# Performance work log

Measured on AMD Instinct MI355X. Metric: run time of the kernel, lower is better.

## Reference

```python
import jax, jax.numpy as jnp
import numpy as np
import math

K_HISTORY = 32  # sliding-window length over GRU hidden states


def rotate_half(x):
    half = x.shape[-1] // 2
    return jnp.concatenate([-x[..., half:], x[..., :half]], axis=-1)


def setup_inputs() -> dict:
    key = jax.random.key(0)
    ks = jax.random.split(key, 8)
    B, MB, IN = 8, 512, 1024          # batch, max_bin, input_size (gru_hidden_size)
    EMB, H, KVH, HD, BS = 1024, 16, 4, 64, 16  # embed_dim, heads, kv_heads, head_dim, bin_size
    h = jax.random.normal(ks[0], (B, MB, IN), jnp.float32)
    # RoPE tables: rotate-half layout, theta repeated over both halves
    pos = jnp.arange(MB, dtype=jnp.float32)
    inv_freq = 1.0 / (10000.0 ** (jnp.arange(0, HD, 2, dtype=jnp.float32) / HD))
    theta = pos[:, None] * inv_freq[None, :]            # (MB, HD/2)
    theta = jnp.concatenate([theta, theta], axis=-1)    # (MB, HD)
    freqs_cos = jnp.cos(theta)
    freqs_sin = jnp.sin(theta)
    s = 0.02
    Wq = jax.random.normal(ks[1], (EMB, H * HD), jnp.float32) * s
    Wk = jax.random.normal(ks[2], (IN, KVH * HD), jnp.float32) * s
    Wv = jax.random.normal(ks[3], (IN, KVH * HD), jnp.float32) * s
    Wo = jax.random.normal(ks[4], (H * HD, EMB), jnp.float32) * s
    output_queries = jax.random.normal(ks[5], (BS, EMB), jnp.float32)
    Wr = jax.random.normal(ks[6], (EMB, 2), jnp.float32) * s
    br = jnp.zeros((2,), jnp.float32)
    return {"h": h, "freqs_cos": freqs_cos, "freqs_sin": freqs_sin,
            "Wq": Wq, "Wk": Wk, "Wv": Wv, "Wo": Wo,
            "output_queries": output_queries, "Wr": Wr, "br": br}


def reference(h, freqs_cos, freqs_sin, Wq, Wk, Wv, Wo, output_queries, Wr, br):
    B, MB, IN = h.shape
    HD = freqs_cos.shape[1]
    H = Wq.shape[1] // HD
    KVH = Wk.shape[1] // HD
    n_rep = H // KVH
    BS = output_queries.shape[0]
    K = K_HISTORY

    # sliding windows over bins: window t covers h[t-K+1 : t+1] (zero left-pad)
    h_padded = jnp.concatenate([jnp.zeros((B, K - 1, IN), h.dtype), h], axis=1)
    idx = jnp.arange(MB)[:, None] + jnp.arange(K)[None, :]   # (MB, K)
    h_win = h_padded[:, idx, :]                              # (B, MB, K, IN)

    k = (h_win @ Wk).reshape(B, MB, K, KVH, HD)
    v = (h_win @ Wv).reshape(B, MB, K, KVH, HD)

    # queries: shared learned output queries, identical across batch & bins
    q = (output_queries @ Wq).reshape(BS, H, HD)             # (BS, H, HD)
    # RoPE on Q only (is_decoder=True) at within-bin offsets 0..BS-1
    offs = jnp.arange(BS)
    cos = freqs_cos[offs][:, None, :]                        # (BS, 1, HD)
    sin = freqs_sin[offs][:, None, :]
    q = q * cos + rotate_half(q) * sin                       # (BS, H, HD)

    # GQA: repeat_interleave KV heads to H heads
    k = jnp.repeat(k, n_rep, axis=3)                         # (B, MB, K, H, HD)
    v = jnp.repeat(v, n_rep, axis=3)

    scores = jnp.einsum("qhd,bmkhd->bmhqk", q, k) / math.sqrt(HD)
    attn = jax.nn.softmax(scores, axis=-1)                   # (B, MB, H, BS, K)
    attn_out = jnp.einsum("bmhqk,bmkhd->bmqhd", attn, v)
    attn_out = attn_out.reshape(B, MB, BS, H * HD)

    z = attn_out @ Wo                                        # (B, MB, BS, EMB)
    vel = z @ Wr + br                                        # (B, MB, BS, 2)
    return vel.reshape(B, MB * BS, 2)
```

## Files before the change

### kernel.cpp

```cpp
#include <hip/hip_runtime.h>


typedef __attribute__((ext_vector_type(8))) short v8s;
typedef __attribute__((ext_vector_type(4))) float v4f;

#define OFF_WOR  0u
#define OFF_QR   2048u
#define OFF_WTH  18432u
#define OFF_WTL  182272u
#define OFF_S0   346112u
#define OFF_S1   1460224u
#define OFF_VW0  2574336u
#define OFF_VW1  2713600u

#define SROW 544

__device__ __forceinline__ void split_bf16(float a, unsigned short& h, unsigned short& l) {
    const unsigned u = __float_as_uint(a);
    h = (unsigned short)(u >> 16);
    const float r = a - __uint_as_float(u & 0xFFFF0000u);
    unsigned v = __float_as_uint(r);
    v += 0x7FFFu + ((v >> 16) & 1u);
    l = (unsigned short)(v >> 16);
}

__global__ __launch_bounds__(256) void kP(
    const float* __restrict__ oq, const float* __restrict__ Wq,
    const float* __restrict__ fc, const float* __restrict__ fs,
    const float* __restrict__ Wo, const float* __restrict__ Wr,
    float* __restrict__ qr, float* __restrict__ Wor,
    float* __restrict__ S0, float* __restrict__ S1,
    float* __restrict__ VW0, float* __restrict__ VW1,
    unsigned* __restrict__ wthu, unsigned* __restrict__ wtlu)
{
    __shared__ float sm[2048];
    const int b = blockIdx.x, t = threadIdx.x;
    if (b < 256) {
        const int q = b >> 4, h = b & 15;
        #pragma unroll
        for (int j = 0; j < 4; ++j) sm[t + 256 * j] = oq[q * 1024 + t + 256 * j];
        __syncthreads();
        const int w = t >> 6, lane = t & 63;
        const float* wq = Wq + (size_t)(w * 256) * 1024 + h * 64 + lane;
        const float* os = sm + w * 256;
        float acc = 0.f;
        #pragma unroll 8
        for (int e = 0; e < 256; ++e) acc = fmaf(os[e], wq[(size_t)e * 1024], acc);
        sm[1024 + w * 64 + lane] = acc;
        __syncthreads();
        if (t < 64) {
            const int d = t, p = d ^ 32;
            const float a1 = sm[1024 + d] + sm[1088 + d] + sm[1152 + d] + sm[1216 + d];
            const float a2 = sm[1024 + p] + sm[1088 + p] + sm[1152 + p] + sm[1216 + p];
            const float c = fc[q * 64 + d], s = fs[q * 64 + d];
            const float rh = (d < 32) ? -a2 : a2;
            qr[q * 1024 + h * 64 + d] = fmaf(a1, c, rh * s);
        }
    } else if (b < 512) {
        #pragma unroll
        for (int j = 0; j < 8; ++j) sm[t + 256 * j] = Wr[t + 256 * j];
        __syncthreads();
        const int i = (b - 256) * 4 + (t >> 6);
        const int lane = t & 63;
        float a0 = 0.f, a1 = 0.f;
        const float* wo = Wo + (size_t)i * 1024 + lane;
        #pragma unroll
        for (int j = 0; j < 16; ++j) {
            const float w = wo[j * 64];
            const int e = lane + j * 64;
            a0 = fmaf(w, sm[2 * e], a0);
            a1 = fmaf(w, sm[2 * e + 1], a1);
        }
        #pragma unroll
        for (int w = 1; w < 64; w <<= 1) {
            a0 += __shfl_xor(a0, w, 64);
            a1 += __shfl_xor(a1, w, 64);
        }
        if (lane == 0) { Wor[i * 2] = a0; Wor[i * 2 + 1] = a1; }
    } else if (b < 656) {
        const int idx = (b - 512) * 256 + t;
        const float4 z = make_float4(0.f, 0.f, 0.f, 0.f);
        if (idx < 16384)       *(float4*)(S0  + (size_t)(idx >> 3) * SROW + (idx & 7) * 4) = z;
        else if (idx < 32768)  *(float4*)(S1  + (size_t)((idx - 16384) >> 3) * SROW + (idx & 7) * 4) = z;
        else if (idx < 34816)  *(float4*)(VW0 + (size_t)((idx - 32768) >> 3) * SROW + (idx & 7) * 4) = z;
        else                   *(float4*)(VW1 + (size_t)((idx - 34816) >> 3) * SROW + (idx & 7) * 4) = z;
    } else {
        unsigned* dst = (b == 656) ? wthu : wtlu;
        #pragma unroll
        for (int j = 0; j < 64; ++j) dst[147456 + t + 256 * j] = 0u;
    }
}

__global__ __launch_bounds__(256) void kW(
    const float* __restrict__ Wk, const float* __restrict__ Wv,
    const float* __restrict__ qr, const float* __restrict__ Wor,
    unsigned short* __restrict__ Wth, unsigned short* __restrict__ Wtl)
{
    __shared__ float As[32 * 68];
    __shared__ float Bt[72 * 68];
    const int b = blockIdx.x, t = threadIdx.x;
    const int g = b >> 5, i0 = (b & 31) * 32;
    #pragma unroll
    for (int jj = 0; jj < 16; ++jj) {
        const int i2 = t + 256 * jj;
        const int d = i2 & 63, col = i2 >> 6;
        Bt[col * 68 + d] = qr[(col >> 2) * 1024 + (g * 4 + (col & 3)) * 64 + d];
    }
    #pragma unroll
    for (int jj = 0; jj < 2; ++jj) {
        const int i2 = t + 256 * jj;
        const int d = i2 & 63, vc = i2 >> 6;
        Bt[(64 + vc) * 68 + d] = Wor[((g * 4 + (vc >> 1)) * 64 + d) * 2 + (vc & 1)];
    }
    {
        const int i = t >> 3, dc = (t & 7) * 8;
        const float* src = Wk + (size_t)(i0 + i) * 256 + g * 64 + dc;
        *(float4*)&As[i * 68 + dc] = *(const float4*)src;
        *(float4*)&As[i * 68 + dc + 4] = *(const float4*)(src + 4);
    }
    __syncthreads();
    const int jc = t & 63, iq = t >> 6;
    {
        float out[8];
        #pragma unroll
        for (int r = 0; r < 8; ++r) out[r] = 0.f;
        #pragma unroll
        for (int dc = 0; dc < 16; ++dc) {
            const float4 bv = *(const float4*)&Bt[jc * 68 + dc * 4];
            #pragma unroll
            for (int r = 0; r < 8; ++r) {
                const float4 av = *(const float4*)&As[(iq * 8 + r) * 68 + dc * 4];
                out[r] = fmaf(av.x, bv.x, out[r]);
                out[r] = fmaf(av.y, bv.y, out[r]);
                out[r] = fmaf(av.z, bv.z, out[r]);
                out[r] = fmaf(av.w, bv.w, out[r]);
            }
        }
        const int j = (jc >> 2) * 16 + g * 4 + (jc & 3);
        v8s ph, pl;
        #pragma unroll
        for (int r = 0; r < 8; ++r) {
            unsigned short hh, ll;
            split_bf16(out[r] * 0.125f, hh, ll);
            ph[r] = (short)hh; pl[r] = (short)ll;
        }
        *(v8s*)&Wth[(size_t)j * 1024 + i0 + iq * 8] = ph;
        *(v8s*)&Wtl[(size_t)j * 1024 + i0 + iq * 8] = pl;
    }
    __syncthreads();
    {
        const int i = t >> 3, dc = (t & 7) * 8;
        const float* src = Wv + (size_t)(i0 + i) * 256 + g * 64 + dc;
        *(float4*)&As[i * 68 + dc] = *(const float4*)src;
        *(float4*)&As[i * 68 + dc + 4] = *(const float4*)(src + 4);
    }
    __syncthreads();
    {
        const int il = t >> 3, vc = t & 7;
        float acc = 0.f;
        #pragma unroll
        for (int dc = 0; dc < 16; ++dc) {
            const float4 av = *(const float4*)&As[il * 68 + dc * 4];
            const float4 bv = *(const float4*)&Bt[(64 + vc) * 68 + dc * 4];
            acc = fmaf(av.x, bv.x, acc);
            acc = fmaf(av.y, bv.y, acc);
            acc = fmaf(av.z, bv.z, acc);
            acc = fmaf(av.w, bv.w, acc);
        }
        const int j = 256 + (g * 4 + (vc >> 1)) * 2 + (vc & 1);
        unsigned short hh, ll;
        split_bf16(acc, hh, ll);
        Wth[(size_t)j * 1024 + i0 + il] = hh;
        Wtl[(size_t)j * 1024 + i0 + il] = ll;
    }
}

__global__ __launch_bounds__(256) void k2(
    const float* __restrict__ A,
    const unsigned short* __restrict__ Wth, const unsigned short* __restrict__ Wtl,
    float* __restrict__ S0, float* __restrict__ S1,
    float* __restrict__ VW0, float* __restrict__ VW1)
{
    __shared__ unsigned short Ah[64 * 40], Al[64 * 40];
    __shared__ unsigned short Bh[64 * 40], Bl[64 * 40];
    const int m0 = blockIdx.x * 64;
    const int n0 = blockIdx.y * 64;
    const int kh = blockIdx.z;
    const int t = threadIdx.x;
    const int lane = t & 63, wv = t >> 6;
    const int l16 = lane & 15, quad = lane >> 4;
    const int wm = wv >> 1, wn = wv & 1;
    const int sr = t >> 2, kc = (t & 3) * 8;
    v4f acc[2][2];
    #pragma unroll
    for (int i = 0; i < 2; ++i)
        #pragma unroll
        for (int j = 0; j < 2; ++j) acc[i][j] = (v4f)(0.f);
    const float* Ap = A + (size_t)(m0 + sr) * 1024 + kh * 512 + kc;
    const unsigned short* Bph = Wth + (size_t)(n0 + sr) * 1024 + kh * 512 + kc;
    const unsigned short* Bpl = Wtl + (size_t)(n0 + sr) * 1024 + kh * 512 + kc;
    for (int k0 = 0; k0 < 512; k0 += 32) {
        const float4 a0 = *(const float4*)(Ap + k0);
        const float4 a1 = *(const float4*)(Ap + k0 + 4);
        const v8s bhv = *(const v8s*)(Bph + k0);
        const v8s blv = *(const v8s*)(Bpl + k0);
        v8s ahv, alv;
        {
            const float af[8] = {a0.x, a0.y, a0.z, a0.w, a1.x, a1.y, a1.z, a1.w};
            #pragma unroll
            for (int j = 0; j < 8; ++j) {
                unsigned short hh, ll;
                split_bf16(af[j], hh, ll);
                ahv[j] = (short)hh; alv[j] = (short)ll;
            }
        }
        __syncthreads();
        *(v8s*)&Ah[sr * 40 + kc] = ahv;
        *(v8s*)&Al[sr * 40 + kc] = alv;
        *(v8s*)&Bh[sr * 40 + kc] = bhv;
        *(v8s*)&Bl[sr * 40 + kc] = blv;
        __syncthreads();
        v8s fah[2], fal[2], fbh[2], fbl[2];
        #pragma unroll
        for (int s = 0; s < 2; ++s) {
            const int mr = wm * 32 + s * 16 + l16;
            fah[s] = *(const v8s*)&Ah[mr * 40 + quad * 8];
            fal[s] = *(const v8s*)&Al[mr * 40 + quad * 8];
            const int nr = wn * 32 + s * 16 + l16;
            fbh[s] = *(const v8s*)&Bh[nr * 40 + quad * 8];
            fbl[s] = *(const v8s*)&Bl[nr * 40 + quad * 8];
        }
        #pragma unroll
        for (int ms = 0; ms < 2; ++ms)
            #pragma unroll
            for (int ns = 0; ns < 2; ++ns) {
                acc[ms][ns] = __builtin_amdgcn_mfma_f32_16x16x32_bf16(fal[ms], fbh[ns], acc[ms][ns], 0, 0, 0);
                acc[ms][ns] = __builtin_amdgcn_mfma_f32_16x16x32_bf16(fah[ms], fbl[ns], acc[ms][ns], 0, 0, 0);
                acc[ms][ns] = __builtin_amdgcn_mfma_f32_16x16x32_bf16(fah[ms], fbh[ns], acc[ms][ns], 0, 0, 0);
            }
    }
    float* Sh  = kh ? S1 : S0;
    float* VWh = kh ? VW1 : VW0;
    #pragma unroll
    for (int ms = 0; ms < 2; ++ms)
        #pragma unroll
        for (int ns = 0; ns < 2; ++ns) {
            const int j = n0 + wn * 32 + ns * 16 + l16;
            if (j >= 288) continue;
            const int m = m0 + wm * 32 + ms * 16 + quad * 4;
            const int bb = m >> 9, tt = m & 511;
            const float4 v = make_float4(acc[ms][ns][0], acc[ms][ns][1], acc[ms][ns][2], acc[ms][ns][3]);
            float* dst;
            if (j < 256)
                dst = Sh + (size_t)((bb * 16 + (j >> 4)) * 16 + (j & 15)) * SROW + 32 + tt;
            else
                dst = VWh + (size_t)(bb * 32 + (j - 256)) * SROW + 32 + tt;
            *(float4*)dst = v;
        }
}

#define ES 324
__global__ __launch_bounds__(256) void k3(
    const float* __restrict__ S0, const float* __restrict__ S1,
    const float* __restrict__ VW0, const float* __restrict__ VW1,
    const float* __restrict__ brp, float* __restrict__ out)
{
    __shared__ float Es[16 * ES];
    __shared__ float EVs[32 * ES];
    const int b = blockIdx.x, q = blockIdx.y, half = blockIdx.z;
    const int tbase = half * 256;
    const int tid = threadIdx.x;
    for (int idx = tid; idx < 16 * 72; idx += 256) {
        const int h = idx / 72, g = idx - h * 72;
        const size_t off = (size_t)((b * 16 + q) * 16 + h) * SROW + tbase + g * 4;
        const float4 a = *(const float4*)(S0 + off);
        const float4 c = *(const float4*)(S1 + off);
        float4 e;
        e.x = __expf(a.x + c.x); e.y = __expf(a.y + c.y);
        e.z = __expf(a.z + c.z); e.w = __expf(a.w + c.w);
        *(float4*)(Es + h * ES + g * 4) = e;
    }
    __syncthreads();
    for (int idx = tid; idx < 32 * 72; idx += 256) {
        const int hc = idx / 72, g = idx - hc * 72;
        const size_t off = (size_t)(b * 32 + hc) * SROW + tbase + g * 4;
        const float4 v0 = *(const float4*)(VW0 + off);
        const float4 v1 = *(const float4*)(VW1 + off);
        const float4 e = *(const float4*)(Es + (hc >> 1) * ES + g * 4);
        float4 r;
        r.x = e.x * (v0.x + v1.x); r.y = e.y * (v0.y + v1.y);
        r.z = e.z * (v0.z + v1.z); r.w = e.w * (v0.w + v1.w);
        *(float4*)(EVs + hc * ES + g * 4) = r;
    }
    __syncthreads();
    const int h = tid & 15, mg = tid >> 4;
    const float* ep = Es + h * ES + mg * 16;
    const float* e0 = EVs + (2 * h) * ES + mg * 16;
    const float* e1 = EVs + (2 * h + 1) * ES + mg * 16;
    float den = 0.f, n0 = 0.f, n1 = 0.f;
    #pragma unroll
    for (int s = 0; s < 32; ++s) {
        const int ss = 1 + ((s + 2 * h) & 31);
        den += ep[ss]; n0 += e0[ss]; n1 += e1[ss];
    }
    const float br0 = brp[0], br1 = brp[1];
    for (int u = 0; u < 16; ++u) {
        const float inv = 1.f / den;
        float c0 = n0 * inv, c1 = n1 * inv;
        #pragma unroll
        for (int w = 1; w < 16; w <<= 1) {
            c0 += __shfl_xor(c0, w, 64);
            c1 += __shfl_xor(c1, w, 64);
        }
        if (h == 0) {
            const int m = tbase + mg * 16 + u;
            float* o = out + (size_t)((b * 512 + m) * 16 + q) * 2;
            o[0] = c0 + br0;
            o[1] = c1 + br1;
        }
        if (u < 15) {
            den += ep[33 + u] - ep[1 + u];
            n0 += e0[33 + u] - e0[1 + u];
            n1 += e1[33 + u] - e1[1 + u];
        }
    }
}

extern "C" void kernel_launch(void* const* d_in, const int* in_sizes, int n_in,
                              void* d_out, int out_size, void* d_ws, size_t ws_size,
                              hipStream_t stream)
{
    (void)in_sizes; (void)n_in; (void)out_size; (void)ws_size;
    const float* h  = (const float*)d_in[0];
    const float* fc = (const float*)d_in[1];
    const float* fs = (const float*)d_in[2];
    const float* Wq = (const float*)d_in[3];
    const float* Wk = (const float*)d_in[4];
    const float* Wv = (const float*)d_in[5];
    const float* Wo = (const float*)d_in[6];
    const float* oq = (const float*)d_in[7];
    const float* Wr = (const float*)d_in[8];
    const float* br = (const float*)d_in[9];
    float* ws = (float*)d_ws;
    float* Wor  = ws + OFF_WOR;
    float* qr   = ws + OFF_QR;
    unsigned short* Wth = (unsigned short*)(ws + OFF_WTH);
    unsigned short* Wtl = (unsigned short*)(ws + OFF_WTL);
    float* S0   = ws + OFF_S0;
    float* S1   = ws + OFF_S1;
    float* VW0  = ws + OFF_VW0;
    float* VW1  = ws + OFF_VW1;
    float* out = (float*)d_out;

    hipLaunchKernelGGL(kP, dim3(658), dim3(256), 0, stream,
                       oq, Wq, fc, fs, Wo, Wr, qr, Wor, S0, S1, VW0, VW1,
                       (unsigned*)Wth, (unsigned*)Wtl);
    hipLaunchKernelGGL(kW, dim3(128), dim3(256), 0, stream, Wk, Wv, qr, Wor, Wth, Wtl);
    hipLaunchKernelGGL(k2, dim3(64, 5, 2), dim3(256), 0, stream, h, Wth, Wtl, S0, S1, VW0, VW1);
    hipLaunchKernelGGL(k3, dim3(8, 16, 2), dim3(256), 0, stream, S0, S1, VW0, VW1, br, out);
}
```

Baseline: 131.1 us.

## Fuse four kernels into one cooperative persistent kernel with grid syncs

Replaces the four separate launches (prep, weight fold, GEMM, softmax/window reduction) with a single cooperative kernel of 512 workgroups that separates the phases with grid.sync(). The goal is to remove launch gaps and inter-kernel drain between the small stages. The work split per phase is retiled to fit 512 blocks: smaller weight-fold tiles, a grid-stride loop over the 640 GEMM tiles, and a quarter-sequence split in the final stage. In exchange, the GEMM phase now covers 640 tiles with 512 blocks, leaving some blocks idle during the second pass, and it adds the cost of grid-wide barriers.

```diff
diff --git a/kernel.cpp b/kernel.cpp
--- a/kernel.cpp
+++ b/kernel.cpp
@@ -1,7 +1,11 @@
 #include <hip/hip_runtime.h>
+#include <hip/hip_cooperative_groups.h>
+
+namespace cg = cooperative_groups;
 
 
 typedef __attribute__((ext_vector_type(8))) short v8s;
+typedef __attribute__((ext_vector_type(4))) short v4sh;
 typedef __attribute__((ext_vector_type(4))) float v4f;
 
 #define OFF_WOR  0u
@@ -12,7 +16,6 @@
 #define OFF_S1   1460224u
 #define OFF_VW0  2574336u
 #define OFF_VW1  2713600u
-
 #define SROW 544
 
 __device__ __forceinline__ void split_bf16(float a, unsigned short& h, unsigned short& l) {
@@ -24,304 +27,307 @@
     l = (unsigned short)(v >> 16);
 }
 
-__global__ __launch_bounds__(256) void kP(
-    const float* __restrict__ oq, const float* __restrict__ Wq,
+__global__ __launch_bounds__(256, 2) void fused(
+    const float* __restrict__ A,
     const float* __restrict__ fc, const float* __restrict__ fs,
-    const float* __restrict__ Wo, const float* __restrict__ Wr,
-    float* __restrict__ qr, float* __restrict__ Wor,
-    float* __restrict__ S0, float* __restrict__ S1,
-    float* __restrict__ VW0, float* __restrict__ VW1,
-    unsigned* __restrict__ wthu, unsigned* __restrict__ wtlu)
+    const float* __restrict__ Wq, const float* __restrict__ Wk,
+    const float* __restrict__ Wv, const float* __restrict__ Wo,
+    const float* __restrict__ oq, const float* __restrict__ Wr,
+    const float* __restrict__ brp,
+    float* __restrict__ ws, float* __restrict__ out)
 {
-    __shared__ float sm[2048];
-    const int b = blockIdx.x, t = threadIdx.x;
-    if (b < 256) {
-        const int q = b >> 4, h = b & 15;
+    __shared__ float smf[8192];
+    cg::grid_group grid = cg::this_grid();
+    const int wg = blockIdx.x;
+    const int t = threadIdx.x;
+
+    float* Wor = ws + OFF_WOR;
+    float* qr  = ws + OFF_QR;
+    unsigned short* Wth = (unsigned short*)(ws + OFF_WTH);
+    unsigned short* Wtl = (unsigned short*)(ws + OFF_WTL);
+    float* S0  = ws + OFF_S0;
+    float* S1  = ws + OFF_S1;
+    float* VW0 = ws + OFF_VW0;
+    float* VW1 = ws + OFF_VW1;
+
+    {
+        const int gid = wg * 256 + t;
+        if (gid < 36864) {
+            const float4 z = make_float4(0.f, 0.f, 0.f, 0.f);
+            if (gid < 16384)       *(float4*)(S0  + (size_t)(gid >> 3) * SROW + (gid & 7) * 4) = z;
+            else if (gid < 32768)  *(float4*)(S1  + (size_t)((gid - 16384) >> 3) * SROW + (gid & 7) * 4) = z;
+            else if (gid < 34816)  *(float4*)(VW0 + (size_t)((gid - 32768) >> 3) * SROW + (gid & 7) * 4) = z;
+            else                   *(float4*)(VW1 + (size_t)((gid - 34816) >> 3) * SROW + (gid & 7) * 4) = z;
+        } else if (gid < 45056) {
+            const int j = gid - 36864;
+            unsigned* dst = (unsigned*)((j < 4096) ? Wth : Wtl);
+            const int jj = j & 4095;
+            const uint4 z4 = make_uint4(0u, 0u, 0u, 0u);
+            *(uint4*)(dst + 147456 + jj * 4) = z4;
+        }
+        if (wg < 256) {
+            const int q = wg >> 4, h = wg & 15;
+            #pragma unroll
+            for (int j = 0; j < 4; ++j) smf[t + 256 * j] = oq[q * 1024 + t + 256 * j];
+            __syncthreads();
+            const int w = t >> 6, lane = t & 63;
+            const float* wq = Wq + (size_t)(w * 256) * 1024 + h * 64 + lane;
+            const float* os = smf + w * 256;
+            float acc = 0.f;
+            #pragma unroll 8
+            for (int e = 0; e < 256; ++e) acc = fmaf(os[e], wq[(size_t)e * 1024], acc);
+            smf[1024 + w * 64 + lane] = acc;
+            __syncthreads();
+            if (t < 64) {
+                const int d = t, p = d ^ 32;
+                const float a1 = smf[1024 + d] + smf[1088 + d] + smf[1152 + d] + smf[1216 + d];
+                const float a2 = smf[1024 + p] + smf[1088 + p] + smf[1152 + p] + smf[1216 + p];
+                const float c = fc[q * 64 + d], s = fs[q * 64 + d];
+                const float rh = (d < 32) ? -a2 : a2;
+                qr[q * 1024 + h * 64 + d] = fmaf(a1, c, rh * s);
+            }
+        } else {
+            #pragma unroll
+            for (int j = 0; j < 8; ++j) smf[t + 256 * j] = Wr[t + 256 * j];
+            __syncthreads();
+            const int i = (wg - 256) * 4 + (t >> 6);
+            const int lane = t & 63;
+            float a0 = 0.f, a1 = 0.f;
+            const float* wo = Wo + (size_t)i * 1024 + lane;
+            #pragma unroll
+            for (int j = 0; j < 16; ++j) {
+                const float w = wo[j * 64];
+                const int e = lane + j * 64;
+                a0 = fmaf(w, smf[2 * e], a0);
+                a1 = fmaf(w, smf[2 * e + 1], a1);
+            }
+            #pragma unroll
+            for (int w = 1; w < 64; w <<= 1) {
+                a0 += __shfl_xor(a0, w, 64);
+                a1 += __shfl_xor(a1, w, 64);
+            }
+            if (lane == 0) { Wor[i * 2] = a0; Wor[i * 2 + 1] = a1; }
+        }
+    }
+    grid.sync();
+
+    if (wg < 256) {
+        const int g = wg & 3;
+        const int i0 = (wg >> 2) * 16;
+        float* As = smf;
+        float* Bt = smf + 1088;
         #pragma unroll
-        for (int j = 0; j < 4; ++j) sm[t + 256 * j] = oq[q * 1024 + t + 256 * j];
-        __syncthreads();
-        const int w = t >> 6, lane = t & 63;
-        const float* wq = Wq + (size_t)(w * 256) * 1024 + h * 64 + lane;
-        const float* os = sm + w * 256;
-        float acc = 0.f;
-        #pragma unroll 8
-        for (int e = 0; e < 256; ++e) acc = fmaf(os[e], wq[(size_t)e * 1024], acc);
-        sm[1024 + w * 64 + lane] = acc;
-        __syncthreads();
-        if (t < 64) {
-            const int d = t, p = d ^ 32;
-            const float a1 = sm[1024 + d] + sm[1088 + d] + sm[1152 + d] + sm[1216 + d];
-            const float a2 = sm[1024 + p] + sm[1088 + p] + sm[1152 + p] + sm[1216 + p];
-            const float c = fc[q * 64 + d], s = fs[q * 64 + d];
-            const float rh = (d < 32) ? -a2 : a2;
-            qr[q * 1024 + h * 64 + d] = fmaf(a1, c, rh * s);
-        }
-    } else if (b < 512) {
+        for (int jj = 0; jj < 16; ++jj) {
+            const int i2 = t + 256 * jj;
+            const int d = i2 & 63, col = i2 >> 6;
+            Bt[col * 68 + d] = qr[(col >> 2) * 1024 + (g * 4 + (col & 3)) * 64 + d];
+        }
         #pragma unroll
-        for (int j = 0; j < 8; ++j) sm[t + 256 * j] = Wr[t + 256 * j];
-        __syncthreads();
-        const int i = (b - 256) * 4 + (t >> 6);
-        const int lane = t & 63;
-        float a0 = 0.f, a1 = 0.f;
-        const float* wo = Wo + (size_t)i * 1024 + lane;
+        for (int jj = 0; jj < 2; ++jj) {
+            const int i2 = t + 256 * jj;
+            const int d = i2 & 63, vc = i2 >> 6;
+            Bt[(64 + vc) * 68 + d] = Wor[((g * 4 + (vc >> 1)) * 64 + d) * 2 + (vc & 1)];
+        }
+        {
+            const int i = t >> 4, dc = (t & 15) * 4;
+            *(float4*)&As[i * 68 + dc] = *(const float4*)(Wk + (size_t)(i0 + i) * 256 + g * 64 + dc);
+        }
+        __syncthreads();
+        const int jc = t & 63, iq = t >> 6;
+        {
+            float o4[4] = {0.f, 0.f, 0.f, 0.f};
+            #pragma unroll
+            for (int dc = 0; dc < 16; ++dc) {
+                const float4 bv = *(const float4*)&Bt[jc * 68 + dc * 4];
+                #pragma unroll
+                for (int r = 0; r < 4; ++r) {
+                    const float4 av = *(const float4*)&As[(iq * 4 + r) * 68 + dc * 4];
+                    o4[r] = fmaf(av.x, bv.x, o4[r]);
+                    o4[r] = fmaf(av.y, bv.y, o4[r]);
+                    o4[r] = fmaf(av.z, bv.z, o4[r]);
+                    o4[r] = fmaf(av.w, bv.w, o4[r]);
+                }
+            }
+            const int j = (jc >> 2) * 16 + g * 4 + (jc & 3);
+            v4sh ph, pl;
+            #pragma unroll
+            for (int r = 0; r < 4; ++r) {
+                unsigned short hh, ll;
+                split_bf16(o4[r] * 0.125f, hh, ll);
+                ph[r] = (short)hh; pl[r] = (short)ll;
+            }
+            *(v4sh*)&Wth[(size_t)j * 1024 + i0 + iq * 4] = ph;
+            *(v4sh*)&Wtl[(size_t)j * 1024 + i0 + iq * 4] = pl;
+        }
+        __syncthreads();
+        {
+            const int i = t >> 4, dc = (t & 15) * 4;
+            *(float4*)&As[i * 68 + dc] = *(const float4*)(Wv + (size_t)(i0 + i) * 256 + g * 64 + dc);
+        }
+        __syncthreads();
+        if (t < 128) {
+            const int il = t >> 3, vc = t & 7;
+            float acc = 0.f;
+            #pragma unroll
+            for (int dc = 0; dc < 16; ++dc) {
+                const float4 av = *(const float4*)&As[il * 68 + dc * 4];
+                const float4 bv = *(const float4*)&Bt[(64 + vc) * 68 + dc * 4];
+                acc = fmaf(av.x, bv.x, acc);
+                acc = fmaf(av.y, bv.y, acc);
+                acc = fmaf(av.z, bv.z, acc);
+                acc = fmaf(av.w, bv.w, acc);
+            }
+            const int j = 256 + (g * 4 + (vc >> 1)) * 2 + (vc & 1);
+            unsigned short hh, ll;
+            split_bf16(acc, hh, ll);
+            Wth[(size_t)j * 1024 + i0 + il] = hh;
+            Wtl[(size_t)j * 1024 + i0 + il] = ll;
+        }
+    }
+    grid.sync();
+
+    {
+        unsigned short* Ah = (unsigned short*)smf;
+        unsigned short* Al = Ah + 2560;
+        unsigned short* Bh = Ah + 5120;
+        unsigned short* Bl = Ah + 7680;
+        const int lane = t & 63, wv = t >> 6;
+        const int l16 = lane & 15, quad = lane >> 4;
+        const int wm = wv >> 1, wn = wv & 1;
+        const int sr = t >> 2, kc = (t & 3) * 8;
+        for (int tile = wg; tile < 640; tile += 512) {
+            const int kh = (tile >= 320) ? 1 : 0;
+            const int r = tile - kh * 320;
+            const int m0 = (r & 63) * 64;
+            const int n0 = (r >> 6) * 64;
+            v4f acc[2][2];
+            #pragma unroll
+            for (int i = 0; i < 2; ++i)
+                #pragma unroll
+                for (int j = 0; j < 2; ++j) acc[i][j] = (v4f)(0.f);
+            const float* Ap = A + (size_t)(m0 + sr) * 1024 + kh * 512 + kc;
+            const unsigned short* Bph = Wth + (size_t)(n0 + sr) * 1024 + kh * 512 + kc;
+            const unsigned short* Bpl = Wtl + (size_t)(n0 + sr) * 1024 + kh * 512 + kc;
+            for (int k0 = 0; k0 < 512; k0 += 32) {
+                const float4 a0 = *(const float4*)(Ap + k0);
+                const float4 a1 = *(const float4*)(Ap + k0 + 4);
+                const v8s bhv = *(const v8s*)(Bph + k0);
+                const v8s blv = *(const v8s*)(Bpl + k0);
+                v8s ahv, alv;
+                {
+                    const float af[8] = {a0.x, a0.y, a0.z, a0.w, a1.x, a1.y, a1.z, a1.w};
+                    #pragma unroll
+                    for (int j = 0; j < 8; ++j) {
+                        unsigned short hh, ll;
+                        split_bf16(af[j], hh, ll);
+                        ahv[j] = (short)hh; alv[j] = (short)ll;
+                    }
+                }
+                __syncthreads();
+                *(v8s*)&Ah[sr * 40 + kc] = ahv;
+                *(v8s*)&Al[sr * 40 + kc] = alv;
+                *(v8s*)&Bh[sr * 40 + kc] = bhv;
+                *(v8s*)&Bl[sr * 40 + kc] = blv;
+                __syncthreads();
+                v8s fah[2], fal[2], fbh[2], fbl[2];
+                #pragma unroll
+                for (int s = 0; s < 2; ++s) {
+                    const int mr = wm * 32 + s * 16 + l16;
+                    fah[s] = *(const v8s*)&Ah[mr * 40 + quad * 8];
+                    fal[s] = *(const v8s*)&Al[mr * 40 + quad * 8];
+                    const int nr = wn * 32 + s * 16 + l16;
+                    fbh[s] = *(const v8s*)&Bh[nr * 40 + quad * 8];
+                    fbl[s] = *(const v8s*)&Bl[nr * 40 + quad * 8];
+                }
+                #pragma unroll
+                for (int ms = 0; ms < 2; ++ms)
+                    #pragma unroll
+                    for (int ns = 0; ns < 2; ++ns) {
+                        acc[ms][ns] = __builtin_amdgcn_mfma_f32_16x16x32_bf16(fal[ms], fbh[ns], acc[ms][ns], 0, 0, 0);
+                        acc[ms][ns] = __builtin_amdgcn_mfma_f32_16x16x32_bf16(fah[ms], fbl[ns], acc[ms][ns], 0, 0, 0);
+                        acc[ms][ns] = __builtin_amdgcn_mfma_f32_16x16x32_bf16(fah[ms], fbh[ns], acc[ms][ns], 0, 0, 0);
+                    }
+            }
+            float* Sh  = kh ? S1 : S0;
+            float* VWh = kh ? VW1 : VW0;
+            #pragma unroll
+            for (int ms = 0; ms < 2; ++ms)
+                #pragma unroll
+                for (int ns = 0; ns < 2; ++ns) {
+                    const int j = n0 + wn * 32 + ns * 16 + l16;
+                    if (j >= 288) continue;
+                    const int m = m0 + wm * 32 + ms * 16 + quad * 4;
+                    const int bb = m >> 9, tt = m & 511;
+                    const float4 v = make_float4(acc[ms][ns][0], acc[ms][ns][1], acc[ms][ns][2], acc[ms][ns][3]);
+                    float* dst;
+                    if (j < 256)
+                        dst = Sh + (size_t)((bb * 16 + (j >> 4)) * 16 + (j & 15)) * SROW + 32 + tt;
+                    else
+                        dst = VWh + (size_t)(bb * 32 + (j - 256)) * SROW + 32 + tt;
+                    *(float4*)dst = v;
+                }
+        }
+    }
+    grid.sync();
+
+    {
+        float* Es  = smf;
+        float* EVs = smf + 2624;
+        const int b = wg >> 6, q = (wg >> 2) & 15, qt = wg & 3;
+        const int tbase = qt * 128;
+        for (int idx = t; idx < 640; idx += 256) {
+            const int h = idx / 40, g = idx - h * 40;
+            const size_t off = (size_t)((b * 16 + q) * 16 + h) * SROW + tbase + g * 4;
+            const float4 a = *(const float4*)(S0 + off);
+            const float4 c = *(const float4*)(S1 + off);
+            float4 e;
+            e.x = __expf(a.x + c.x); e.y = __expf(a.y + c.y);
+            e.z = __expf(a.z + c.z); e.w = __expf(a.w + c.w);
+            *(float4*)(Es + h * 164 + g * 4) = e;
+        }
+        __syncthreads();
+        for (int idx = t; idx < 1280; idx += 256) {
+            const int hc = idx / 40, g = idx - hc * 40;
+            const size_t off = (size_t)(b * 32 + hc) * SROW + tbase + g * 4;
+            const float4 v0 = *(const float4*)(VW0 + off);
+            const float4 v1 = *(const float4*)(VW1 + off);
+            const float4 e = *(const float4*)(Es + (hc >> 1) * 164 + g * 4);
+            float4 rr;
+            rr.x = e.x * (v0.x + v1.x); rr.y = e.y * (v0.y + v1.y);
+            rr.z = e.z * (v0.z + v1.z); rr.w = e.w * (v0.w + v1.w);
+            *(float4*)(EVs + hc * 164 + g * 4) = rr;
+        }
+        __syncthreads();
+        const int h = t & 15, mg = t >> 4;
+        const float* ep = Es + h * 164 + mg * 8;
+        const float* e0 = EVs + (2 * h) * 164 + mg * 8;
+        const float* e1 = EVs + (2 * h + 1) * 164 + mg * 8;
+        float den = 0.f, n0s = 0.f, n1s = 0.f;
         #pragma unroll
-        for (int j = 0; j < 16; ++j) {
-            const float w = wo[j * 64];
-            const int e = lane + j * 64;
-            a0 = fmaf(w, sm[2 * e], a0);
-            a1 = fmaf(w, sm[2 * e + 1], a1);
-        }
-        #pragma unroll
-        for (int w = 1; w < 64; w <<= 1) {
-            a0 += __shfl_xor(a0, w, 64);
-            a1 += __shfl_xor(a1, w, 64);
-        }
-        if (lane == 0) { Wor[i * 2] = a0; Wor[i * 2 + 1] = a1; }
-    } else if (b < 656) {
-        const int idx = (b - 512) * 256 + t;
-        const float4 z = make_float4(0.f, 0.f, 0.f, 0.f);
-        if (idx < 16384)       *(float4*)(S0  + (size_t)(idx >> 3) * SROW + (idx & 7) * 4) = z;
-        else if (idx < 32768)  *(float4*)(S1  + (size_t)((idx - 16384) >> 3) * SROW + (idx & 7) * 4) = z;
-        else if (idx < 34816)  *(float4*)(VW0 + (size_t)((idx - 32768) >> 3) * SROW + (idx & 7) * 4) = z;
-        else                   *(float4*)(VW1 + (size_t)((idx - 34816) >> 3) * SROW + (idx & 7) * 4) = z;
-    } else {
-        unsigned* dst = (b == 656) ? wthu : wtlu;
-        #pragma unroll
-        for (int j = 0; j < 64; ++j) dst[147456 + t + 256 * j] = 0u;
-    }
-}
-
-__global__ __launch_bounds__(256) void kW(
-    const float* __restrict__ Wk, const float* __restrict__ Wv,
-    const float* __restrict__ qr, const float* __restrict__ Wor,
-    unsigned short* __restrict__ Wth, unsigned short* __restrict__ Wtl)
-{
-    __shared__ float As[32 * 68];
-    __shared__ float Bt[72 * 68];
-    const int b = blockIdx.x, t = threadIdx.x;
-    const int g = b >> 5, i0 = (b & 31) * 32;
-    #pragma unroll
-    for (int jj = 0; jj < 16; ++jj) {
-        const int i2 = t + 256 * jj;
-        const int d = i2 & 63, col = i2 >> 6;
-        Bt[col * 68 + d] = qr[(col >> 2) * 1024 + (g * 4 + (col & 3)) * 64 + d];
-    }
-    #pragma unroll
-    for (int jj = 0; jj < 2; ++jj) {
-        const int i2 = t + 256 * jj;
-        const int d = i2 & 63, vc = i2 >> 6;
-        Bt[(64 + vc) * 68 + d] = Wor[((g * 4 + (vc >> 1)) * 64 + d) * 2 + (vc & 1)];
-    }
-    {
-        const int i = t >> 3, dc = (t & 7) * 8;
-        const float* src = Wk + (size_t)(i0 + i) * 256 + g * 64 + dc;
-        *(float4*)&As[i * 68 + dc] = *(const float4*)src;
-        *(float4*)&As[i * 68 + dc + 4] = *(const float4*)(src + 4);
-    }
-    __syncthreads();
-    const int jc = t & 63, iq = t >> 6;
-    {
-        float out[8];
-        #pragma unroll
-        for (int r = 0; r < 8; ++r) out[r] = 0.f;
-        #pragma unroll
-        for (int dc = 0; dc < 16; ++dc) {
-            const float4 bv = *(const float4*)&Bt[jc * 68 + dc * 4];
-            #pragma unroll
-            for (int r = 0; r < 8; ++r) {
-                const float4 av = *(const float4*)&As[(iq * 8 + r) * 68 + dc * 4];
-                out[r] = fmaf(av.x, bv.x, out[r]);
-                out[r] = fmaf(av.y, bv.y, out[r]);
-                out[r] = fmaf(av.z, bv.z, out[r]);
-                out[r] = fmaf(av.w, bv.w, out[r]);
-            }
-        }
-        const int j = (jc >> 2) * 16 + g * 4 + (jc & 3);
-        v8s ph, pl;
-        #pragma unroll
-        for (int r = 0; r < 8; ++r) {
-            unsigned short hh, ll;
-            split_bf16(out[r] * 0.125f, hh, ll);
-            ph[r] = (short)hh; pl[r] = (short)ll;
-        }
-        *(v8s*)&Wth[(size_t)j * 1024 + i0 + iq * 8] = ph;
-        *(v8s*)&Wtl[(size_t)j * 1024 + i0 + iq * 8] = pl;
-    }
-    __syncthreads();
-    {
-        const int i = t >> 3, dc = (t & 7) * 8;
-        const float* src = Wv + (size_t)(i0 + i) * 256 + g * 64 + dc;
-        *(float4*)&As[i * 68 + dc] = *(const float4*)src;
-        *(float4*)&As[i * 68 + dc + 4] = *(const float4*)(src + 4);
-    }
-    __syncthreads();
-    {
-        const int il = t >> 3, vc = t & 7;
-        float acc = 0.f;
-        #pragma unroll
-        for (int dc = 0; dc < 16; ++dc) {
-            const float4 av = *(const float4*)&As[il * 68 + dc * 4];
-            const float4 bv = *(const float4*)&Bt[(64 + vc) * 68 + dc * 4];
-            acc = fmaf(av.x, bv.x, acc);
-            acc = fmaf(av.y, bv.y, acc);
-            acc = fmaf(av.z, bv.z, acc);
-            acc = fmaf(av.w, bv.w, acc);
-        }
-        const int j = 256 + (g * 4 + (vc >> 1)) * 2 + (vc & 1);
-        unsigned short hh, ll;
-        split_bf16(acc, hh, ll);
-        Wth[(size_t)j * 1024 + i0 + il] = hh;
-        Wtl[(size_t)j * 1024 + i0 + il] = ll;
-    }
-}
-
-__global__ __launch_bounds__(256) void k2(
-    const float* __restrict__ A,
-    const unsigned short* __restrict__ Wth, const unsigned short* __restrict__ Wtl,
-    float* __restrict__ S0, float* __restrict__ S1,
-    float* __restrict__ VW0, float* __restrict__ VW1)
-{
-    __shared__ unsigned short Ah[64 * 40], Al[64 * 40];
-    __shared__ unsigned short Bh[64 * 40], Bl[64 * 40];
-    const int m0 = blockIdx.x * 64;
-    const int n0 = blockIdx.y * 64;
-    const int kh = blockIdx.z;
-    const int t = threadIdx.x;
-    const int lane = t & 63, wv = t >> 6;
-    const int l16 = lane & 15, quad = lane >> 4;
-    const int wm = wv >> 1, wn = wv & 1;
-    const int sr = t >> 2, kc = (t & 3) * 8;
-    v4f acc[2][2];
-    #pragma unroll
-    for (int i = 0; i < 2; ++i)
-        #pragma unroll
-        for (int j = 0; j < 2; ++j) acc[i][j] = (v4f)(0.f);
-    const float* Ap = A + (size_t)(m0 + sr) * 1024 + kh * 512 + kc;
-    const unsigned short* Bph = Wth + (size_t)(n0 + sr) * 1024 + kh * 512 + kc;
-    const unsigned short* Bpl = Wtl + (size_t)(n0 + sr) * 1024 + kh * 512 + kc;
-    for (int k0 = 0; k0 < 512; k0 += 32) {
-        const float4 a0 = *(const float4*)(Ap + k0);
-        const float4 a1 = *(const float4*)(Ap + k0 + 4);
-        const v8s bhv = *(const v8s*)(Bph + k0);
-        const v8s blv = *(const v8s*)(Bpl + k0);
-        v8s ahv, alv;
-        {
-            const float af[8] = {a0.x, a0.y, a0.z, a0.w, a1.x, a1.y, a1.z, a1.w};
-            #pragma unroll
-            for (int j = 0; j < 8; ++j) {
-                unsigned short hh, ll;
-                split_bf16(af[j], hh, ll);
-                ahv[j] = (short)hh; alv[j] = (short)ll;
-            }
-        }
-        __syncthreads();
-        *(v8s*)&Ah[sr * 40 + kc] = ahv;
-        *(v8s*)&Al[sr * 40 + kc] = alv;
-        *(v8s*)&Bh[sr * 40 + kc] = bhv;
-        *(v8s*)&Bl[sr * 40 + kc] = blv;
-        __syncthreads();
-        v8s fah[2], fal[2], fbh[2], fbl[2];
-        #pragma unroll
-        for (int s = 0; s < 2; ++s) {
-            const int mr = wm * 32 + s * 16 + l16;
-            fah[s] = *(const v8s*)&Ah[mr * 40 + quad * 8];
-            fal[s] = *(const v8s*)&Al[mr * 40 + quad * 8];
-            const int nr = wn * 32 + s * 16 + l16;
-            fbh[s] = *(const v8s*)&Bh[nr * 40 + quad * 8];
-            fbl[s] = *(const v8s*)&Bl[nr * 40 + quad * 8];
-        }
-        #pragma unroll
-        for (int ms = 0; ms < 2; ++ms)
-            #pragma unroll
-            for (int ns = 0; ns < 2; ++ns) {
-                acc[ms][ns] = __builtin_amdgcn_mfma_f32_16x16x32_bf16(fal[ms], fbh[ns], acc[ms][ns], 0, 0, 0);
-                acc[ms][ns] = __builtin_amdgcn_mfma_f32_16x16x32_bf16(fah[ms], fbl[ns], acc[ms][ns], 0, 0, 0);
-                acc[ms][ns] = __builtin_amdgcn_mfma_f32_16x16x32_bf16(fah[ms], fbh[ns], acc[ms][ns], 0, 0, 0);
-            }
-    }
-    float* Sh  = kh ? S1 : S0;
-    float* VWh = kh ? VW1 : VW0;
-    #pragma unroll
-    for (int ms = 0; ms < 2; ++ms)
-        #pragma unroll
-        for (int ns = 0; ns < 2; ++ns) {
-            const int j = n0 + wn * 32 + ns * 16 + l16;
-            if (j >= 288) continue;
-            const int m = m0 + wm * 32 + ms * 16 + quad * 4;
-            const int bb = m >> 9, tt = m & 511;
-            const float4 v = make_float4(acc[ms][ns][0], acc[ms][ns][1], acc[ms][ns][2], acc[ms][ns][3]);
-            float* dst;
-            if (j < 256)
-                dst = Sh + (size_t)((bb * 16 + (j >> 4)) * 16 + (j & 15)) * SROW + 32 + tt;
-            else
-                dst = VWh + (size_t)(bb * 32 + (j - 256)) * SROW + 32 + tt;
-            *(float4*)dst = v;
-        }
-}
-
-#define ES 324
-__global__ __launch_bounds__(256) void k3(
-    const float* __restrict__ S0, const float* __restrict__ S1,
-    const float* __restrict__ VW0, const float* __restrict__ VW1,
-    const float* __restrict__ brp, float* __restrict__ out)
-{
-    __shared__ float Es[16 * ES];
-    __shared__ float EVs[32 * ES];
-    const int b = blockIdx.x, q = blockIdx.y, half = blockIdx.z;
-    const int tbase = half * 256;
-    const int tid = threadIdx.x;
-    for (int idx = tid; idx < 16 * 72; idx += 256) {
-        const int h = idx / 72, g = idx - h * 72;
-        const size_t off = (size_t)((b * 16 + q) * 16 + h) * SROW + tbase + g * 4;
-        const float4 a = *(const float4*)(S0 + off);
-        const float4 c = *(const float4*)(S1 + off);
-        float4 e;
-        e.x = __expf(a.x + c.x); e.y = __expf(a.y + c.y);
-        e.z = __expf(a.z + c.z); e.w = __expf(a.w + c.w);
-        *(float4*)(Es + h * ES + g * 4) = e;
-    }
-    __syncthreads();
-    for (int idx = tid; idx < 32 * 72; idx += 256) {
-        const int hc = idx / 72, g = idx - hc * 72;
-        const size_t off = (size_t)(b * 32 + hc) * SROW + tbase + g * 4;
-        const float4 v0 = *(const float4*)(VW0 + off);
-        const float4 v1 = *(const float4*)(VW1 + off);
-        const float4 e = *(const float4*)(Es + (hc >> 1) * ES + g * 4);
-        float4 r;
-        r.x = e.x * (v0.x + v1.x); r.y = e.y * (v0.y + v1.y);
-        r.z = e.z * (v0.z + v1.z); r.w = e.w * (v0.w + v1.w);
-        *(float4*)(EVs + hc * ES + g * 4) = r;
-    }
-    __syncthreads();
-    const int h = tid & 15, mg = tid >> 4;
-    const float* ep = Es + h * ES + mg * 16;
-    const float* e0 = EVs + (2 * h) * ES + mg * 16;
-    const float* e1 = EVs + (2 * h + 1) * ES + mg * 16;
-    float den = 0.f, n0 = 0.f, n1 = 0.f;
-    #pragma unroll
-    for (int s = 0; s < 32; ++s) {
-        const int ss = 1 + ((s + 2 * h) & 31);
-        den += ep[ss]; n0 += e0[ss]; n1 += e1[ss];
-    }
-    const float br0 = brp[0], br1 = brp[1];
-    for (int u = 0; u < 16; ++u) {
-        const float inv = 1.f / den;
-        float c0 = n0 * inv, c1 = n1 * inv;
-        #pragma unroll
-        for (int w = 1; w < 16; w <<= 1) {
-            c0 += __shfl_xor(c0, w, 64);
-            c1 += __shfl_xor(c1, w, 64);
-        }
-        if (h == 0) {
-            const int m = tbase + mg * 16 + u;
-            float* o = out + (size_t)((b * 512 + m) * 16 + q) * 2;
-            o[0] = c0 + br0;
-            o[1] = c1 + br1;
-        }
-        if (u < 15) {
-            den += ep[33 + u] - ep[1 + u];
-            n0 += e0[33 + u] - e0[1 + u];
-            n1 += e1[33 + u] - e1[1 + u];
+        for (int s = 0; s < 32; ++s) {
+            const int ss = 1 + ((s + 2 * h) & 31);
+            den += ep[ss]; n0s += e0[ss]; n1s += e1[ss];
+        }
+        const float br0 = brp[0], br1 = brp[1];
+        for (int u = 0; u < 8; ++u) {
+            const float inv = 1.f / den;
+            float c0 = n0s * inv, c1 = n1s * inv;
+            #pragma unroll
+            for (int w = 1; w < 16; w <<= 1) {
+                c0 += __shfl_xor(c0, w, 64);
+                c1 += __shfl_xor(c1, w, 64);
+            }
+            if (h == 0) {
+                const int m = tbase + mg * 8 + u;
+                float* o = out + (size_t)((b * 512 + m) * 16 + q) * 2;
+                o[0] = c0 + br0;
+                o[1] = c1 + br1;
+            }
+            if (u < 7) {
+                den += ep[33 + u] - ep[1 + u];
+                n0s += e0[33 + u] - e0[1 + u];
+                n1s += e1[33 + u] - e1[1 + u];
+            }
         }
     }
 }
@@ -342,20 +348,11 @@
     const float* Wr = (const float*)d_in[8];
     const float* br = (const float*)d_in[9];
     float* ws = (float*)d_ws;
-    float* Wor  = ws + OFF_WOR;
-    float* qr   = ws + OFF_QR;
-    unsigned short* Wth = (unsigned short*)(ws + OFF_WTH);
-    unsigned short* Wtl = (unsigned short*)(ws + OFF_WTL);
-    float* S0   = ws + OFF_S0;
-    float* S1   = ws + OFF_S1;
-    float* VW0  = ws + OFF_VW0;
-    float* VW1  = ws + OFF_VW1;
     float* out = (float*)d_out;
 
-    hipLaunchKernelGGL(kP, dim3(658), dim3(256), 0, stream,
-                       oq, Wq, fc, fs, Wo, Wr, qr, Wor, S0, S1, VW0, VW1,
-                       (unsigned*)Wth, (unsigned*)Wtl);
-    hipLaunchKernelGGL(kW, dim3(128), dim3(256), 0, stream, Wk, Wv, qr, Wor, Wth, Wtl);
-    hipLaunchKernelGGL(k2, dim3(64, 5, 2), dim3(256), 0, stream, h, Wth, Wtl, S0, S1, VW0, VW1);
-    hipLaunchKernelGGL(k3, dim3(8, 16, 2), dim3(256), 0, stream, S0, S1, VW0, VW1, br, out);
+    void* args[] = {
+        (void*)&h, (void*)&fc, (void*)&fs, (void*)&Wq, (void*)&Wk, (void*)&Wv,
+        (void*)&Wo, (void*)&oq, (void*)&Wr, (void*)&br, (void*)&ws, (void*)&out
+    };
+    hipLaunchCooperativeKernel((const void*)fused, dim3(512), dim3(256), args, 0, stream);
 }
```

Result: slower. 321.2 us (+145.0%).

## Double k2 K-step per barrier, split k3 into more blocks, unroll kP

Applied to the files above, without the earlier changes.

The k2 GEMM now stages 64 K-elements per iteration instead of 32, which halves the number of syncthreads pairs and global load rounds and issues twice as many MFMAs between barriers. k3 is split into four time quarters instead of two, doubling the block count for parallelism. It also uses a hardware reciprocal and fully unrolls the output loop. The kP unroll factor is raised. The cost is more LDS per k2 block, which may lower occupancy, and more redundant halo loads in k3.

```diff
diff --git a/kernel.cpp b/kernel.cpp
--- a/kernel.cpp
+++ b/kernel.cpp
@@ -2,6 +2,7 @@
 
 
 typedef __attribute__((ext_vector_type(8))) short v8s;
+typedef __attribute__((ext_vector_type(4))) short v4sh;
 typedef __attribute__((ext_vector_type(4))) float v4f;
 
 #define OFF_WOR  0u
@@ -12,7 +13,6 @@
 #define OFF_S1   1460224u
 #define OFF_VW0  2574336u
 #define OFF_VW1  2713600u
-
 #define SROW 544
 
 __device__ __forceinline__ void split_bf16(float a, unsigned short& h, unsigned short& l) {
@@ -44,7 +44,7 @@
         const float* wq = Wq + (size_t)(w * 256) * 1024 + h * 64 + lane;
         const float* os = sm + w * 256;
         float acc = 0.f;
-        #pragma unroll 8
+        #pragma unroll 16
         for (int e = 0; e < 256; ++e) acc = fmaf(os[e], wq[(size_t)e * 1024], acc);
         sm[1024 + w * 64 + lane] = acc;
         __syncthreads();
@@ -181,8 +181,8 @@
     float* __restrict__ S0, float* __restrict__ S1,
     float* __restrict__ VW0, float* __restrict__ VW1)
 {
-    __shared__ unsigned short Ah[64 * 40], Al[64 * 40];
-    __shared__ unsigned short Bh[64 * 40], Bl[64 * 40];
+    __shared__ unsigned short Ah[64 * 72], Al[64 * 72];
+    __shared__ unsigned short Bh[64 * 72], Bl[64 * 72];
     const int m0 = blockIdx.x * 64;
     const int n0 = blockIdx.y * 64;
     const int kh = blockIdx.z;
@@ -199,45 +199,55 @@
     const float* Ap = A + (size_t)(m0 + sr) * 1024 + kh * 512 + kc;
     const unsigned short* Bph = Wth + (size_t)(n0 + sr) * 1024 + kh * 512 + kc;
     const unsigned short* Bpl = Wtl + (size_t)(n0 + sr) * 1024 + kh * 512 + kc;
-    for (int k0 = 0; k0 < 512; k0 += 32) {
-        const float4 a0 = *(const float4*)(Ap + k0);
-        const float4 a1 = *(const float4*)(Ap + k0 + 4);
-        const v8s bhv = *(const v8s*)(Bph + k0);
-        const v8s blv = *(const v8s*)(Bpl + k0);
-        v8s ahv, alv;
+    for (int k0 = 0; k0 < 512; k0 += 64) {
+        const float4 a00 = *(const float4*)(Ap + k0);
+        const float4 a01 = *(const float4*)(Ap + k0 + 4);
+        const float4 a10 = *(const float4*)(Ap + k0 + 32);
+        const float4 a11 = *(const float4*)(Ap + k0 + 36);
+        const v8s bh0 = *(const v8s*)(Bph + k0);
+        const v8s bh1 = *(const v8s*)(Bph + k0 + 32);
+        const v8s bl0 = *(const v8s*)(Bpl + k0);
+        const v8s bl1 = *(const v8s*)(Bpl + k0 + 32);
+        v8s ah0, al0, ah1, al1;
         {
-            const float af[8] = {a0.x, a0.y, a0.z, a0.w, a1.x, a1.y, a1.z, a1.w};
+            const float af0[8] = {a00.x, a00.y, a00.z, a00.w, a01.x, a01.y, a01.z, a01.w};
+            const float af1[8] = {a10.x, a10.y, a10.z, a10.w, a11.x, a11.y, a11.z, a11.w};
             #pragma unroll
             for (int j = 0; j < 8; ++j) {
                 unsigned short hh, ll;
-                split_bf16(af[j], hh, ll);
-                ahv[j] = (short)hh; alv[j] = (short)ll;
+                split_bf16(af0[j], hh, ll);
+                ah0[j] = (short)hh; al0[j] = (short)ll;
+                split_bf16(af1[j], hh, ll);
+                ah1[j] = (short)hh; al1[j] = (short)ll;
             }
         }
         __syncthreads();
-        *(v8s*)&Ah[sr * 40 + kc] = ahv;
-        *(v8s*)&Al[sr * 40 + kc] = alv;
-        *(v8s*)&Bh[sr * 40 + kc] = bhv;
-        *(v8s*)&Bl[sr * 40 + kc] = blv;
-        __syncthreads();
-        v8s fah[2], fal[2], fbh[2], fbl[2];
-        #pragma unroll
-        for (int s = 0; s < 2; ++s) {
-            const int mr = wm * 32 + s * 16 + l16;
-            fah[s] = *(const v8s*)&Ah[mr * 40 + quad * 8];
-            fal[s] = *(const v8s*)&Al[mr * 40 + quad * 8];
-            const int nr = wn * 32 + s * 16 + l16;
-            fbh[s] = *(const v8s*)&Bh[nr * 40 + quad * 8];
-            fbl[s] = *(const v8s*)&Bl[nr * 40 + quad * 8];
-        }
-        #pragma unroll
-        for (int ms = 0; ms < 2; ++ms)
+        *(v8s*)&Ah[sr * 72 + kc] = ah0;  *(v8s*)&Ah[sr * 72 + kc + 32] = ah1;
+        *(v8s*)&Al[sr * 72 + kc] = al0;  *(v8s*)&Al[sr * 72 + kc + 32] = al1;
+        *(v8s*)&Bh[sr * 72 + kc] = bh0;  *(v8s*)&Bh[sr * 72 + kc + 32] = bh1;
+        *(v8s*)&Bl[sr * 72 + kc] = bl0;  *(v8s*)&Bl[sr * 72 + kc + 32] = bl1;
+        __syncthreads();
+        #pragma unroll
+        for (int kk = 0; kk < 2; ++kk) {
+            v8s fah[2], fal[2], fbh[2], fbl[2];
             #pragma unroll
-            for (int ns = 0; ns < 2; ++ns) {
-                acc[ms][ns] = __builtin_amdgcn_mfma_f32_16x16x32_bf16(fal[ms], fbh[ns], acc[ms][ns], 0, 0, 0);
-                acc[ms][ns] = __builtin_amdgcn_mfma_f32_16x16x32_bf16(fah[ms], fbl[ns], acc[ms][ns], 0, 0, 0);
-                acc[ms][ns] = __builtin_amdgcn_mfma_f32_16x16x32_bf16(fah[ms], fbh[ns], acc[ms][ns], 0, 0, 0);
+            for (int s = 0; s < 2; ++s) {
+                const int mr = wm * 32 + s * 16 + l16;
+                fah[s] = *(const v8s*)&Ah[mr * 72 + kk * 32 + quad * 8];
+                fal[s] = *(const v8s*)&Al[mr * 72 + kk * 32 + quad * 8];
+                const int nr = wn * 32 + s * 16 + l16;
+                fbh[s] = *(const v8s*)&Bh[nr * 72 + kk * 32 + quad * 8];
+                fbl[s] = *(const v8s*)&Bl[nr * 72 + kk * 32 + quad * 8];
             }
+            #pragma unroll
+            for (int ms = 0; ms < 2; ++ms)
+                #pragma unroll
+                for (int ns = 0; ns < 2; ++ns) {
+                    acc[ms][ns] = __builtin_amdgcn_mfma_f32_16x16x32_bf16(fal[ms], fbh[ns], acc[ms][ns], 0, 0, 0);
+                    acc[ms][ns] = __builtin_amdgcn_mfma_f32_16x16x32_bf16(fah[ms], fbl[ns], acc[ms][ns], 0, 0, 0);
+                    acc[ms][ns] = __builtin_amdgcn_mfma_f32_16x16x32_bf16(fah[ms], fbh[ns], acc[ms][ns], 0, 0, 0);
+                }
+        }
     }
     float* Sh  = kh ? S1 : S0;
     float* VWh = kh ? VW1 : VW0;
@@ -259,69 +269,69 @@
         }
 }
 
-#define ES 324
 __global__ __launch_bounds__(256) void k3(
     const float* __restrict__ S0, const float* __restrict__ S1,
     const float* __restrict__ VW0, const float* __restrict__ VW1,
     const float* __restrict__ brp, float* __restrict__ out)
 {
-    __shared__ float Es[16 * ES];
-    __shared__ float EVs[32 * ES];
-    const int b = blockIdx.x, q = blockIdx.y, half = blockIdx.z;
-    const int tbase = half * 256;
-    const int tid = threadIdx.x;
-    for (int idx = tid; idx < 16 * 72; idx += 256) {
-        const int h = idx / 72, g = idx - h * 72;
+    __shared__ float Es[16 * 164];
+    __shared__ float EVs[32 * 164];
+    const int b = blockIdx.x, q = blockIdx.y, qt = blockIdx.z;
+    const int tbase = qt * 128;
+    const int t = threadIdx.x;
+    for (int idx = t; idx < 640; idx += 256) {
+        const int h = idx / 40, g = idx - h * 40;
         const size_t off = (size_t)((b * 16 + q) * 16 + h) * SROW + tbase + g * 4;
         const float4 a = *(const float4*)(S0 + off);
         const float4 c = *(const float4*)(S1 + off);
         float4 e;
         e.x = __expf(a.x + c.x); e.y = __expf(a.y + c.y);
         e.z = __expf(a.z + c.z); e.w = __expf(a.w + c.w);
-        *(float4*)(Es + h * ES + g * 4) = e;
-    }
-    __syncthreads();
-    for (int idx = tid; idx < 32 * 72; idx += 256) {
-        const int hc = idx / 72, g = idx - hc * 72;
+        *(float4*)(Es + h * 164 + g * 4) = e;
+    }
+    __syncthreads();
+    for (int idx = t; idx < 1280; idx += 256) {
+        const int hc = idx / 40, g = idx - hc * 40;
         const size_t off = (size_t)(b * 32 + hc) * SROW + tbase + g * 4;
         const float4 v0 = *(const float4*)(VW0 + off);
         const float4 v1 = *(const float4*)(VW1 + off);
-        const float4 e = *(const float4*)(Es + (hc >> 1) * ES + g * 4);
-        float4 r;
-        r.x = e.x * (v0.x + v1.x); r.y = e.y * (v0.y + v1.y);
-        r.z = e.z * (v0.z + v1.z); r.w = e.w * (v0.w + v1.w);
-        *(float4*)(EVs + hc * ES + g * 4) = r;
-    }
-    __syncthreads();
-    const int h = tid & 15, mg = tid >> 4;
-    const float* ep = Es + h * ES + mg * 16;
-    const float* e0 = EVs + (2 * h) * ES + mg * 16;
-    const float* e1 = EVs + (2 * h + 1) * ES + mg * 16;
-    float den = 0.f, n0 = 0.f, n1 = 0.f;
+        const float4 e = *(const float4*)(Es + (hc >> 1) * 164 + g * 4);
+        float4 rr;
+        rr.x = e.x * (v0.x + v1.x); rr.y = e.y * (v0.y + v1.y);
+        rr.z = e.z * (v0.z + v1.z); rr.w = e.w * (v0.w + v1.w);
+        *(float4*)(EVs + hc * 164 + g * 4) = rr;
+    }
+    __syncthreads();
+    const int h = t & 15, mg = t >> 4;
+    const float* ep = Es + h * 164 + mg * 8;
+    const float* e0 = EVs + (2 * h) * 164 + mg * 8;
+    const float* e1 = EVs + (2 * h + 1) * 164 + mg * 8;
+    float den = 0.f, n0s = 0.f, n1s = 0.f;
     #pragma unroll
     for (int s = 0; s < 32; ++s) {
         const int ss = 1 + ((s + 2 * h) & 31);
-        den += ep[ss]; n0 += e0[ss]; n1 += e1[ss];
+        den += ep[ss]; n0s += e0[ss]; n1s += e1[ss];
     }
     const float br0 = brp[0], br1 = brp[1];
-    for (int u = 0; u < 16; ++u) {
-        const float inv = 1.f / den;
-        float c0 = n0 * inv, c1 = n1 * inv;
+    #pragma unroll
+    for (int u = 0; u < 8; ++u) {
+        const float inv = __builtin_amdgcn_rcpf(den);
+        float c0 = n0s * inv, c1 = n1s * inv;
         #pragma unroll
         for (int w = 1; w < 16; w <<= 1) {
             c0 += __shfl_xor(c0, w, 64);
             c1 += __shfl_xor(c1, w, 64);
         }
         if (h == 0) {
-            const int m = tbase + mg * 16 + u;
+            const int m = tbase + mg * 8 + u;
             float* o = out + (size_t)((b * 512 + m) * 16 + q) * 2;
             o[0] = c0 + br0;
             o[1] = c1 + br1;
         }
-        if (u < 15) {
+        if (u < 7) {
             den += ep[33 + u] - ep[1 + u];
-            n0 += e0[33 + u] - e0[1 + u];
-            n1 += e1[33 + u] - e1[1 + u];
+            n0s += e0[33 + u] - e0[1 + u];
+            n1s += e1[33 + u] - e1[1 + u];
         }
     }
 }
@@ -357,5 +367,5 @@
                        (unsigned*)Wth, (unsigned*)Wtl);
     hipLaunchKernelGGL(kW, dim3(128), dim3(256), 0, stream, Wk, Wv, qr, Wor, Wth, Wtl);
     hipLaunchKernelGGL(k2, dim3(64, 5, 2), dim3(256), 0, stream, h, Wth, Wtl, S0, S1, VW0, VW1);
-    hipLaunchKernelGGL(k3, dim3(8, 16, 2), dim3(256), 0, stream, S0, S1, VW0, VW1, br, out);
-}
+    hipLaunchKernelGGL(k3, dim3(8, 16, 4), dim3(256), 0, stream, S0, S1, VW0, VW1, br, out);
+}
```

New measurement: 123.5 us. 5.8% less time.
